# Performance work log

Hardware: AMD Instinct MI355X
Metric: run time of the kernel (lower is better)

Reference implementation:

```python
import jax, jax.numpy as jnp
import numpy as np

B, N, D_IN, D_OUT, K_NBR = 8, 2048, 128, 128, 8
BN_EPS = 1e-5

def setup_inputs() -> dict:
    key = jax.random.key(0)
    ks = jax.random.split(key, 5)
    xavier = (6.0 / (D_IN + D_OUT)) ** 0.5
    return {
        "x": jax.random.normal(ks[0], (B, N, D_IN), jnp.float32),
        "weight_self": jax.random.uniform(ks[1], (D_IN, D_OUT), jnp.float32, -xavier, xavier),
        "weight_neighbor": jax.random.uniform(ks[2], (D_IN, D_OUT), jnp.float32, -xavier, xavier),
        "kan_a": jax.random.normal(ks[3], (D_OUT, 3), jnp.float32) * 0.1,
        "kan_b": jax.random.normal(ks[4], (D_OUT, 2), jnp.float32) * 0.1,
        "bias": jnp.zeros((D_OUT,), jnp.float32),
        "bn_gamma": jnp.ones((D_OUT,), jnp.float32),
        "bn_beta": jnp.zeros((D_OUT,), jnp.float32),
    }

def _forward(x, weight_self, weight_neighbor, kan_a, kan_b, bias, bn_gamma, bn_beta):
    b, n, _ = x.shape
    # --- kNN graph build ---
    xx = jnp.sum(x * x, axis=2, keepdims=True)                       # [B,N,1]
    dist = xx - 2.0 * jnp.einsum('bnd,bmd->bnm', x, x) + jnp.swapaxes(xx, 1, 2)
    dist = jnp.clip(dist, 0.0, None)                                  # [B,N,N]
    k = min(K_NBR + 1, n)
    _, idx = jax.lax.top_k(-dist, k)                                  # smallest-k indices
    nbr = idx[:, :, 1:]                                               # drop self, [B,N,k-1]
    adj = jnp.zeros((b, n, n), x.dtype).at[
        jnp.arange(b)[:, None, None], jnp.arange(n)[None, :, None], nbr
    ].set(1.0)
    deg_inv_sqrt = (jnp.sum(adj, axis=2) + 1e-6) ** -0.5              # [B,N]
    adj_norm = deg_inv_sqrt[:, :, None] * adj * deg_inv_sqrt[:, None, :]
    adj_norm = adj_norm + jnp.eye(n, dtype=x.dtype)[None]
    # --- graph conv ---
    h_self = x @ weight_self                                          # [B,N,F]
    h_nbr = jnp.einsum('bnm,bmf->bnf', adj_norm, x @ weight_neighbor)
    h = h_self + h_nbr + bias
    # --- rational KAN activation (per-channel coefficients) ---
    h2 = h * h
    num = kan_a[:, 0] + kan_a[:, 1] * h + kan_a[:, 2] * h2
    den = 1.0 + jnp.abs(kan_b[:, 0] * h + kan_b[:, 1] * h2)
    h = num / (den + 1e-8)
    # --- BatchNorm1d (training mode): normalize each channel over (B,N) ---
    mean = jnp.mean(h, axis=(0, 1))
    var = jnp.var(h, axis=(0, 1))                                     # biased, matches torch BN
    h = (h - mean) * jax.lax.rsqrt(var + BN_EPS) * bn_gamma + bn_beta
    return h

def reference(x, weight_self, weight_neighbor, kan_a, kan_b, bias, bn_gamma, bn_beta):
    return _forward(x, weight_self, weight_neighbor, kan_a, kan_b, bias, bn_gamma, bn_beta)
```

## Files before the change

kernel.cpp:

```cpp
#include <hip/hip_runtime.h>
#include <stdint.h>

#define BB 8
#define NN 2048
#define DD 128

typedef unsigned long long ull;
typedef unsigned int u32;
typedef unsigned short u16;
typedef __attribute__((ext_vector_type(8))) short bf16x8;
typedef __attribute__((ext_vector_type(4))) float f32x4;

#define INS8(t8, cand) do { \
    t8[7] = (cand); ull _t; \
    if (t8[7] < t8[6]) { _t = t8[6]; t8[6] = t8[7]; t8[7] = _t; } \
    if (t8[6] < t8[5]) { _t = t8[5]; t8[5] = t8[6]; t8[6] = _t; } \
    if (t8[5] < t8[4]) { _t = t8[4]; t8[4] = t8[5]; t8[5] = _t; } \
    if (t8[4] < t8[3]) { _t = t8[3]; t8[3] = t8[4]; t8[4] = _t; } \
    if (t8[3] < t8[2]) { _t = t8[2]; t8[2] = t8[3]; t8[3] = _t; } \
    if (t8[2] < t8[1]) { _t = t8[1]; t8[1] = t8[2]; t8[2] = _t; } \
    if (t8[1] < t8[0]) { _t = t8[0]; t8[0] = t8[1]; t8[1] = _t; } \
  } while (0)

#define CEX(a, b) do { u32 _lo = (a) < (b) ? (a) : (b); \
                       u32 _hi = (a) < (b) ? (b) : (a); \
                       (a) = _lo; (b) = _hi; } while (0)

#define SORT8(c) do { \
    CEX(c[0], c[1]); CEX(c[2], c[3]); CEX(c[0], c[2]); CEX(c[1], c[3]); CEX(c[1], c[2]); \
    CEX(c[4], c[5]); CEX(c[6], c[7]); CEX(c[4], c[6]); CEX(c[5], c[7]); CEX(c[5], c[6]); \
    CEX(c[0], c[4]); CEX(c[1], c[5]); CEX(c[2], c[6]); CEX(c[3], c[7]); \
    CEX(c[2], c[4]); CEX(c[3], c[5]); \
    CEX(c[1], c[2]); CEX(c[3], c[4]); CEX(c[5], c[6]); } while (0)

#define MERGE8(t, s) do { \
    u32 m0_ = (t)[0] < (s)[7] ? (t)[0] : (s)[7]; \
    u32 m1_ = (t)[1] < (s)[6] ? (t)[1] : (s)[6]; \
    u32 m2_ = (t)[2] < (s)[5] ? (t)[2] : (s)[5]; \
    u32 m3_ = (t)[3] < (s)[4] ? (t)[3] : (s)[4]; \
    u32 m4_ = (t)[4] < (s)[3] ? (t)[4] : (s)[3]; \
    u32 m5_ = (t)[5] < (s)[2] ? (t)[5] : (s)[2]; \
    u32 m6_ = (t)[6] < (s)[1] ? (t)[6] : (s)[1]; \
    u32 m7_ = (t)[7] < (s)[0] ? (t)[7] : (s)[0]; \
    CEX(m0_, m4_); CEX(m1_, m5_); CEX(m2_, m6_); CEX(m3_, m7_); \
    CEX(m0_, m2_); CEX(m1_, m3_); CEX(m4_, m6_); CEX(m5_, m7_); \
    CEX(m0_, m1_); CEX(m2_, m3_); CEX(m4_, m5_); CEX(m6_, m7_); \
    (t)[0] = m0_; (t)[1] = m1_; (t)[2] = m2_; (t)[3] = m3_; \
    (t)[4] = m4_; (t)[5] = m5_; (t)[6] = m6_; (t)[7] = m7_; \
  } while (0)

__device__ inline u16 f2bf_rn(float f) {
  uint32_t u = __float_as_uint(f);
  return (u16)((u + 0x7fffu + ((u >> 16) & 1u)) >> 16);
}

typedef __attribute__((address_space(1))) const void gvoid_t;
typedef __attribute__((address_space(3))) void lvoid_t;
__device__ __forceinline__ void gload16(const void* g, void* l) {
  __builtin_amdgcn_global_load_lds((gvoid_t*)g, (lvoid_t*)l, 16, 0, 0);
}

__global__ __launch_bounds__(256) void k_cvx(const float* __restrict__ x,
                                             float* __restrict__ xx,
                                             u16* __restrict__ xh,
                                             u16* __restrict__ xl) {
  int row  = blockIdx.x * 4 + (threadIdx.x >> 6);
  int lane = threadIdx.x & 63;
  float2 v = *reinterpret_cast<const float2*>(x + (size_t)row * DD + lane * 2);
  float p = v.x * v.x + v.y * v.y;
  #pragma unroll
  for (int off = 1; off < 64; off <<= 1) p += __shfl_xor(p, off);
  if (lane == 0) xx[row] = p;
  u16 h0 = f2bf_rn(v.x);
  u16 l0 = f2bf_rn(v.x - __uint_as_float(((uint32_t)h0) << 16));
  u16 h1 = f2bf_rn(v.y);
  u16 l1 = f2bf_rn(v.y - __uint_as_float(((uint32_t)h1) << 16));
  size_t o = (size_t)row * DD + lane * 2;
  *(uint32_t*)(xh + o) = (uint32_t)h0 | ((uint32_t)h1 << 16);
  *(uint32_t*)(xl + o) = (uint32_t)l0 | ((uint32_t)l1 << 16);
}

__global__ __launch_bounds__(256, 2) void k_gemm(const float* __restrict__ x,
                                                 const float* __restrict__ Ws,
                                                 const float* __restrict__ Wn,
                                                 const float* __restrict__ bias,
                                                 float* __restrict__ hbase,
                                                 float* __restrict__ y) {
  __shared__ __align__(16) float xt[128 * 64];
  __shared__ __align__(16) float wt[128 * 64];
  int tid = threadIdx.x;
  int ch = blockIdx.x & 1;
  size_t r0 = (size_t)(blockIdx.x >> 1) * 64;

  {
    int rr = tid >> 2, kp = (tid & 3) << 5;
    const float* src = x + (r0 + rr) * DD + kp;
    #pragma unroll
    for (int q = 0; q < 8; ++q) {
      float4 v = *(const float4*)(src + (q << 2));
      int k = kp + (q << 2);
      xt[(k + 0) * 64 + rr] = v.x; xt[(k + 1) * 64 + rr] = v.y;
      xt[(k + 2) * 64 + rr] = v.z; xt[(k + 3) * 64 + rr] = v.w;
    }
  }
  {
    const float4* s4 = (const float4*)Ws;
    float4* w4 = (float4*)wt;
    #pragma unroll
    for (int q = 0; q < 8; ++q) {
      int idx = q * 256 + tid;
      w4[idx] = s4[((idx >> 4) << 5) + (ch << 4) + (idx & 15)];
    }
  }
  __syncthreads();

  int tc = tid & 15, tr = tid >> 4;
  float accS[4][4], accY[4][4];
  #pragma unroll
  for (int i = 0; i < 4; ++i)
    #pragma unroll
    for (int u = 0; u < 4; ++u) { accS[i][u] = 0.f; accY[i][u] = 0.f; }

  #pragma unroll 4
  for (int k = 0; k < 128; ++k) {
    float4 a4 = *(const float4*)(xt + k * 64 + (tr << 2));
    float4 w4 = *(const float4*)(wt + k * 64 + (tc << 2));
    float aa[4] = {a4.x, a4.y, a4.z, a4.w};
    float ww[4] = {w4.x, w4.y, w4.z, w4.w};
    #pragma unroll
    for (int i = 0; i < 4; ++i)
      #pragma unroll
      for (int u = 0; u < 4; ++u) accS[i][u] = fmaf(aa[i], ww[u], accS[i][u]);
  }
  __syncthreads();
  {
    const float4* s4 = (const float4*)Wn;
    float4* w4 = (float4*)wt;
    #pragma unroll
    for (int q = 0; q < 8; ++q) {
      int idx = q * 256 + tid;
      w4[idx] = s4[((idx >> 4) << 5) + (ch << 4) + (idx & 15)];
    }
  }
  __syncthreads();
  #pragma unroll 4
  for (int k = 0; k < 128; ++k) {
    float4 a4 = *(const float4*)(xt + k * 64 + (tr << 2));
    float4 w4 = *(const float4*)(wt + k * 64 + (tc << 2));
    float aa[4] = {a4.x, a4.y, a4.z, a4.w};
    float ww[4] = {w4.x, w4.y, w4.z, w4.w};
    #pragma unroll
    for (int i = 0; i < 4; ++i)
      #pragma unroll
      for (int u = 0; u < 4; ++u) accY[i][u] = fmaf(aa[i], ww[u], accY[i][u]);
  }

  int cg = (ch << 6) + (tc << 2);
  float4 bv = *(const float4*)(bias + cg);
  float bb[4] = {bv.x, bv.y, bv.z, bv.w};
  #pragma unroll
  for (int i = 0; i < 4; ++i) {
    size_t row = r0 + (tr << 2) + i;
    float h[4];
    #pragma unroll
    for (int u = 0; u < 4; ++u) h[u] = (accS[i][u] + accY[i][u]) + bb[u];
    *(float4*)(y + row * DD + cg)     = make_float4(accY[i][0], accY[i][1], accY[i][2], accY[i][3]);
    *(float4*)(hbase + row * DD + cg) = make_float4(h[0], h[1], h[2], h[3]);
  }
}

#define GLOAD(MC, BUF) do { \
    _Pragma("unroll") \
    for (int q = 0; q < 4; ++q) { \
      int ks_ = ((q & 1) << 2) + sks; \
      int mrow_ = mbase + ((MC) << 5) + ((q >> 1) << 4) + sr; \
      const u16* src_ = (ks_ < 4 ? xhb : xlb) + ((size_t)mrow_ << 7) + ((ks_ & 3) << 5) + (sg << 3); \
      gload16(src_, (char*)(&Bc[(BUF)][0]) + (((q << 8) + tid) << 4)); \
    } } while (0)

__global__ __launch_bounds__(256, 4) void k_knn(const u16* __restrict__ xh,
                                                const u16* __restrict__ xl,
                                                const float* __restrict__ xx,
                                                u32* __restrict__ cand) {
  __shared__ __align__(16) u16 Bc[2][8192];
  __shared__ float xxm[512];

  int tid = threadIdx.x;
  int lane = tid & 63, w = tid >> 6;
  int b = blockIdx.x & 7;
  int rest = blockIdx.x >> 3;
  int n0 = (rest & 31) << 6;
  int msplit = rest >> 5;
  int mbase = msplit << 9;
  const u16*  xhb = xh + (((size_t)b << 11) << 7);
  const u16*  xlb = xl + (((size_t)b << 11) << 7);
  const float* xxb = xx + ((size_t)b << 11);

  int sr = tid & 15, sg = (tid >> 4) & 3, sks = (tid >> 6) & 3;

  GLOAD(0, 0);

  {
    float2 t = *(const float2*)(xxb + mbase + tid * 2);
    xxm[tid * 2] = t.x; xxm[tid * 2 + 1] = t.y;
  }

  int r = lane & 15, g = lane >> 4;
  int myn = n0 + (w << 4) + r;
  float xxn = xxb[myn];

  bf16x8 ah[4], al[4];
  #pragma unroll
  for (int ks = 0; ks < 4; ++ks) {
    ah[ks] = *(const bf16x8*)(xhb + ((size_t)myn << 7) + (ks << 5) + (g << 3));
    al[ks] = *(const bf16x8*)(xlb + ((size_t)myn << 7) + (ks << 5) + (g << 3));
  }

  u32 t8[8];
  #pragma unroll
  for (int q = 0; q < 8; ++q) t8[q] = 0xFFFFFFFFu;

  __syncthreads();

  int cur = 0;
  for (int mc = 0; mc < 16; ++mc) {
    if (mc < 15) GLOAD(mc + 1, cur ^ 1);
    const u16* Bcur = &Bc[cur][0];
    u32 cds[8];
    #pragma unroll
    for (int p = 0; p < 2; ++p) {
      f32x4 ahh = {0.f, 0.f, 0.f, 0.f};
      f32x4 alh = {0.f, 0.f, 0.f, 0.f};
      f32x4 ahl = {0.f, 0.f, 0.f, 0.f};
      #pragma unroll
      for (int ks = 0; ks < 4; ++ks) {
        const u16* base = Bcur + (((p << 3) + ks) << 9) + (lane << 3);
        bf16x8 bh = *(const bf16x8*)(base);
        bf16x8 bo = *(const bf16x8*)(base + 2048);
        ahh = __builtin_amdgcn_mfma_f32_16x16x32_bf16(bh, ah[ks], ahh, 0, 0, 0);
        alh = __builtin_amdgcn_mfma_f32_16x16x32_bf16(bo, ah[ks], alh, 0, 0, 0);
        ahl = __builtin_amdgcn_mfma_f32_16x16x32_bf16(bh, al[ks], ahl, 0, 0, 0);
      }
      float4 xm4 = *(const float4*)(xxm + (mc << 5) + (p << 4) + (g << 2));
      float sx[4] = {xxn + xm4.x, xxn + xm4.y, xxn + xm4.z, xxn + xm4.w};
      int mb0 = mbase + (mc << 5) + (p << 4) + (g << 2);
      #pragma unroll
      for (int e = 0; e < 4; ++e) {
        float dot = (ahh[e] + alh[e]) + ahl[e];
        float d = fmaxf(fmaf(-2.f, dot, sx[e]), 0.f);
        int m = mb0 + e;
        u32 cd = (__float_as_uint(d) & 0xFFFFF000u) | (u32)m;
        cds[(p << 2) + e] = (m == myn) ? 0xFFFFFFFFu : cd;
      }
    }
    SORT8(cds);
    MERGE8(t8, cds);
    __syncthreads();
    cur ^= 1;
  }

  u32* mbuf = (u32*)(&Bc[0][0]);
  #pragma unroll
  for (int q = 0; q < 8; ++q)
    mbuf[((((w << 4) + r) << 5)) + (g << 3) + q] = t8[q];
  __syncthreads();
  if (g == 0) {
    for (int j = 1; j < 4; ++j) {
      u32 s8[8];
      #pragma unroll
      for (int q = 0; q < 8; ++q)
        s8[q] = mbuf[((((w << 4) + r) << 5)) + (j << 3) + q];
      MERGE8(t8, s8);
    }
    u32* cp = cand + ((((size_t)b << 11) + myn) << 5) + (msplit << 3);
    #pragma unroll
    for (int q = 0; q < 8; ++q) cp[q] = t8[q];
  }
}

__global__ __launch_bounds__(256) void k_rsc(const float* __restrict__ x,
                                             const float* __restrict__ xx,
                                             const u32* __restrict__ cand,
                                             int* __restrict__ nbr) {
  __shared__ ull ex[256];
  int tid = threadIdx.x;
  int rloc = tid >> 5;
  int c = tid & 31;
  int batch = blockIdx.x & 7;
  int within = blockIdx.x >> 3;
  int row = (batch << 11) + (within << 3) + rloc;
  u32 cd32 = cand[((size_t)row << 5) + c];
  int m = (int)(cd32 & 0xFFFu);
  const float* xn = x + (size_t)row * DD;
  const float* xm = x + ((size_t)(batch << 11) + m) * DD;
  float acc[8] = {0.f, 0.f, 0.f, 0.f, 0.f, 0.f, 0.f, 0.f};
  #pragma unroll
  for (int d8 = 0; d8 < 16; ++d8) {
    float4 a0 = *(const float4*)(xn + (d8 << 3));
    float4 a1 = *(const float4*)(xn + (d8 << 3) + 4);
    float4 v0 = *(const float4*)(xm + (d8 << 3));
    float4 v1 = *(const float4*)(xm + (d8 << 3) + 4);
    acc[0] = fmaf(a0.x, v0.x, acc[0]);
    acc[1] = fmaf(a0.y, v0.y, acc[1]);
    acc[2] = fmaf(a0.z, v0.z, acc[2]);
    acc[3] = fmaf(a0.w, v0.w, acc[3]);
    acc[4] = fmaf(a1.x, v1.x, acc[4]);
    acc[5] = fmaf(a1.y, v1.y, acc[5]);
    acc[6] = fmaf(a1.z, v1.z, acc[6]);
    acc[7] = fmaf(a1.w, v1.w, acc[7]);
  }
  float dot = ((acc[0] + acc[1]) + (acc[2] + acc[3])) +
              ((acc[4] + acc[5]) + (acc[6] + acc[7]));
  float dist = fmaxf((xx[row] - 2.f * dot) + xx[(batch << 11) + m], 0.f);
  ex[tid] = (((ull)__float_as_uint(dist)) << 32) | (unsigned)m;
  __syncthreads();
  if (c == 0) {
    ull t8[8];
    #pragma unroll
    for (int q = 0; q < 8; ++q) t8[q] = ~0ull;
    #pragma unroll
    for (int q = 0; q < 32; ++q) {
      ull v = ex[(rloc << 5) + q];
      if (v < t8[7]) INS8(t8, v);
    }
    int* op = nbr + (size_t)row * 8;
    #pragma unroll
    for (int q = 0; q < 8; ++q) op[q] = (int)(t8[q] & 0xffffffffu);
  }
}

__global__ __launch_bounds__(256) void k_kan(const float* __restrict__ hbase,
                                             const float* __restrict__ y,
                                             const int* __restrict__ nbr,
                                             const float* __restrict__ kan_a,
                                             const float* __restrict__ kan_b,
                                             float* __restrict__ hkan,
                                             double* __restrict__ sums) {
  __shared__ double redA[256], redB[256];
  int f = threadIdx.x & 127;
  int half = threadIdx.x >> 7;
  int batch = blockIdx.x & 7;
  int within = blockIdx.x >> 3;
  int r0 = (batch << 11) + (within << 5) + half * 16;
  const float* yb = y + ((size_t)batch << 11) * DD;
  float a0 = kan_a[f * 3 + 0], a1 = kan_a[f * 3 + 1], a2 = kan_a[f * 3 + 2];
  float b0 = kan_b[f * 2 + 0], b1 = kan_b[f * 2 + 1];
  float disf = (float)(1.0 / sqrt((double)(8.0f + 1e-6f)));
  float cf = disf * disf;
  double sh = 0.0, sh2 = 0.0;
  for (int i = 0; i < 16; ++i) {
    int r = r0 + i;
    const int* np_ = nbr + (size_t)r * 8;
    float t = 0.f;
    #pragma unroll
    for (int j = 0; j < 8; ++j) {
      int m = np_[j];
      float yv = yb[(size_t)m * DD + f];
      t = fmaf(cf, yv, t);
    }
    float h = hbase[(size_t)r * DD + f] + t;
    float h2 = h * h;
    float num = (a0 + a1 * h) + a2 * h2;
    float den = 1.0f + fabsf(b0 * h + b1 * h2);
    float hk = num / (den + 1e-8f);
    hkan[(size_t)r * DD + f] = hk;
    sh += (double)hk; sh2 += (double)hk * (double)hk;
  }
  redA[threadIdx.x] = sh; redB[threadIdx.x] = sh2;
  __syncthreads();
  if (half == 0) {
    atomicAdd(&sums[f], sh + redA[f + 128]);
    atomicAdd(&sums[128 + f], sh2 + redB[f + 128]);
  }
}

__global__ __launch_bounds__(256) void k_bn(const float* __restrict__ hkan,
                                            const double* __restrict__ sums,
                                            const float* __restrict__ gamma,
                                            const float* __restrict__ beta,
                                            float* __restrict__ out) {
  __shared__ float mn[128], sc[128], bt[128];
  int tid = threadIdx.x;
  if (tid < 128) {
    double M = (double)(BB * NN);
    double mean = sums[tid] / M;
    double var = sums[128 + tid] / M - mean * mean;
    if (var < 0.0) var = 0.0;
    mn[tid] = (float)mean;
    sc[tid] = (float)(1.0 / sqrt(var + 1e-5)) * gamma[tid];
    bt[tid] = beta[tid];
  }
  __syncthreads();
  const int total4 = BB * NN * DD / 4;
  for (int i4 = blockIdx.x * blockDim.x + threadIdx.x; i4 < total4;
       i4 += gridDim.x * blockDim.x) {
    float4 v = ((const float4*)hkan)[i4];
    int fb = (i4 * 4) & 127;
    float4 o;
    o.x = (v.x - mn[fb + 0]) * sc[fb + 0] + bt[fb + 0];
    o.y = (v.y - mn[fb + 1]) * sc[fb + 1] + bt[fb + 1];
    o.z = (v.z - mn[fb + 2]) * sc[fb + 2] + bt[fb + 2];
    o.w = (v.w - mn[fb + 3]) * sc[fb + 3] + bt[fb + 3];
    ((float4*)out)[i4] = o;
  }
}

extern "C" void kernel_launch(void* const* d_in, const int* in_sizes, int n_in,
                              void* d_out, int out_size, void* d_ws, size_t ws_size,
                              hipStream_t stream) {
  const float* x     = (const float*)d_in[0];
  const float* Ws    = (const float*)d_in[1];
  const float* Wn    = (const float*)d_in[2];
  const float* ka    = (const float*)d_in[3];
  const float* kb    = (const float*)d_in[4];
  const float* bias  = (const float*)d_in[5];
  const float* gamma = (const float*)d_in[6];
  const float* beta  = (const float*)d_in[7];
  float* out = (float*)d_out;

  char* ws = (char*)d_ws;
  float*  xx    = (float*)(ws + 0);
  int*    nbr   = (int*)(ws + 65536);
  double* sums  = (double*)(ws + 589824);
  float*  y     = (float*)(ws + 1048576);
  float*  hbase = (float*)(ws + 9437184);
  float*  hkan  = (float*)(ws + 17825792);
  u32*    cand  = (u32*)(ws + 17825792);
  u16*    xh    = (u16*)(ws + 22020096);
  u16*    xl    = (u16*)d_out;

  hipMemsetAsync(sums, 0, 256 * sizeof(double), stream);
  k_cvx <<<4096, 256, 0, stream>>>(x, xx, xh, xl);
  k_gemm<<<512,  256, 0, stream>>>(x, Ws, Wn, bias, hbase, y);
  k_knn <<<1024, 256, 0, stream>>>(xh, xl, xx, cand);
  k_rsc <<<2048, 256, 0, stream>>>(x, xx, cand, nbr);
  k_kan <<<512,  256, 0, stream>>>(hbase, y, nbr, ka, kb, hkan, sums);
  k_bn  <<<1024, 256, 0, stream>>>(hkan, sums, gamma, beta, out);
}
```

Baseline: 149.2 us.

## Skip sort/merge when tile has no better candidates; rescore only top-16 candidates

In the kNN tile loop, each thread first computes the min of its 8 candidates and only runs the sort-and-merge network when that min can enter the running top-8. The rescore kernel now bitonic-merges the four split lists down to the best 16 approximate candidates, instead of 32, before the exact fp32 rescoring. That halves the rescore grid and its gather traffic. The candidate key keeps 11 bits for the index instead of 12 (N=2048), which gives the distance one more bit of precision. Keeping only 16 candidates risks missing a true neighbour when the approximate distances are nearly tied.

After: 131.8 us. -11.6%, faster.

```diff
diff --git a/kernel.cpp b/kernel.cpp
--- a/kernel.cpp
+++ b/kernel.cpp
@@ -47,6 +47,15 @@
     CEX(m0_, m1_); CEX(m2_, m3_); CEX(m4_, m5_); CEX(m6_, m7_); \
     (t)[0] = m0_; (t)[1] = m1_; (t)[2] = m2_; (t)[3] = m3_; \
     (t)[4] = m4_; (t)[5] = m5_; (t)[6] = m6_; (t)[7] = m7_; \
+  } while (0)
+
+#define BMERGE16(c) do { \
+    _Pragma("unroll") for (int _i = 0; _i < 8; ++_i) CEX(c[_i], c[_i + 8]); \
+    _Pragma("unroll") for (int _g = 0; _g < 16; _g += 8) \
+      _Pragma("unroll") for (int _i = 0; _i < 4; ++_i) CEX(c[_g + _i], c[_g + _i + 4]); \
+    _Pragma("unroll") for (int _g = 0; _g < 16; _g += 4) \
+      _Pragma("unroll") for (int _i = 0; _i < 2; ++_i) CEX(c[_g + _i], c[_g + _i + 2]); \
+    _Pragma("unroll") for (int _g = 0; _g < 16; _g += 2) CEX(c[_g], c[_g + 1]); \
   } while (0)
 
 __device__ inline u16 f2bf_rn(float f) {
@@ -249,12 +258,23 @@
         float dot = (ahh[e] + alh[e]) + ahl[e];
         float d = fmaxf(fmaf(-2.f, dot, sx[e]), 0.f);
         int m = mb0 + e;
-        u32 cd = (__float_as_uint(d) & 0xFFFFF000u) | (u32)m;
+        u32 cd = (__float_as_uint(d) & 0xFFFFF800u) | (u32)m;
         cds[(p << 2) + e] = (m == myn) ? 0xFFFFFFFFu : cd;
       }
     }
-    SORT8(cds);
-    MERGE8(t8, cds);
+    {
+      u32 c01 = cds[0] < cds[1] ? cds[0] : cds[1];
+      u32 c23 = cds[2] < cds[3] ? cds[2] : cds[3];
+      u32 c45 = cds[4] < cds[5] ? cds[4] : cds[5];
+      u32 c67 = cds[6] < cds[7] ? cds[6] : cds[7];
+      u32 c03 = c01 < c23 ? c01 : c23;
+      u32 c47 = c45 < c67 ? c45 : c67;
+      u32 cmin = c03 < c47 ? c03 : c47;
+      if (cmin < t8[7]) {
+        SORT8(cds);
+        MERGE8(t8, cds);
+      }
+    }
     __syncthreads();
     cur ^= 1;
   }
@@ -282,45 +302,65 @@
                                              const float* __restrict__ xx,
                                              const u32* __restrict__ cand,
                                              int* __restrict__ nbr) {
-  __shared__ ull ex[256];
+  __shared__ u32 c16[16][16];
+  __shared__ ull ex[16][16];
   int tid = threadIdx.x;
-  int rloc = tid >> 5;
-  int c = tid & 31;
+  int rloc = tid >> 4;
+  int c = tid & 15;
   int batch = blockIdx.x & 7;
   int within = blockIdx.x >> 3;
-  int row = (batch << 11) + (within << 3) + rloc;
-  u32 cd32 = cand[((size_t)row << 5) + c];
-  int m = (int)(cd32 & 0xFFFu);
-  const float* xn = x + (size_t)row * DD;
-  const float* xm = x + ((size_t)(batch << 11) + m) * DD;
-  float acc[8] = {0.f, 0.f, 0.f, 0.f, 0.f, 0.f, 0.f, 0.f};
-  #pragma unroll
-  for (int d8 = 0; d8 < 16; ++d8) {
-    float4 a0 = *(const float4*)(xn + (d8 << 3));
-    float4 a1 = *(const float4*)(xn + (d8 << 3) + 4);
-    float4 v0 = *(const float4*)(xm + (d8 << 3));
-    float4 v1 = *(const float4*)(xm + (d8 << 3) + 4);
-    acc[0] = fmaf(a0.x, v0.x, acc[0]);
-    acc[1] = fmaf(a0.y, v0.y, acc[1]);
-    acc[2] = fmaf(a0.z, v0.z, acc[2]);
-    acc[3] = fmaf(a0.w, v0.w, acc[3]);
-    acc[4] = fmaf(a1.x, v1.x, acc[4]);
-    acc[5] = fmaf(a1.y, v1.y, acc[5]);
-    acc[6] = fmaf(a1.z, v1.z, acc[6]);
-    acc[7] = fmaf(a1.w, v1.w, acc[7]);
-  }
-  float dot = ((acc[0] + acc[1]) + (acc[2] + acc[3])) +
-              ((acc[4] + acc[5]) + (acc[6] + acc[7]));
-  float dist = fmaxf((xx[row] - 2.f * dot) + xx[(batch << 11) + m], 0.f);
-  ex[tid] = (((ull)__float_as_uint(dist)) << 32) | (unsigned)m;
+  int row = (batch << 11) + (within << 4) + rloc;
+
+  if (c == 0) {
+    const u32* cp = cand + ((size_t)row << 5);
+    u32 A[16], B[16];
+    #pragma unroll
+    for (int q = 0; q < 8; ++q) { A[q] = cp[q];      A[8 + q] = cp[15 - q]; }
+    #pragma unroll
+    for (int q = 0; q < 8; ++q) { B[q] = cp[16 + q]; B[8 + q] = cp[31 - q]; }
+    BMERGE16(A);
+    BMERGE16(B);
+    #pragma unroll
+    for (int i = 0; i < 16; ++i) {
+      u32 lo = A[i] < B[15 - i] ? A[i] : B[15 - i];
+      c16[rloc][i] = lo & 0x7FFu;
+    }
+  }
+  __syncthreads();
+
+  {
+    int m = (int)c16[rloc][c];
+    const float* xn = x + (size_t)row * DD;
+    const float* xm = x + ((size_t)(batch << 11) + m) * DD;
+    float acc[8] = {0.f, 0.f, 0.f, 0.f, 0.f, 0.f, 0.f, 0.f};
+    #pragma unroll
+    for (int d8 = 0; d8 < 16; ++d8) {
+      float4 a0 = *(const float4*)(xn + (d8 << 3));
+      float4 a1 = *(const float4*)(xn + (d8 << 3) + 4);
+      float4 v0 = *(const float4*)(xm + (d8 << 3));
+      float4 v1 = *(const float4*)(xm + (d8 << 3) + 4);
+      acc[0] = fmaf(a0.x, v0.x, acc[0]);
+      acc[1] = fmaf(a0.y, v0.y, acc[1]);
+      acc[2] = fmaf(a0.z, v0.z, acc[2]);
+      acc[3] = fmaf(a0.w, v0.w, acc[3]);
+      acc[4] = fmaf(a1.x, v1.x, acc[4]);
+      acc[5] = fmaf(a1.y, v1.y, acc[5]);
+      acc[6] = fmaf(a1.z, v1.z, acc[6]);
+      acc[7] = fmaf(a1.w, v1.w, acc[7]);
+    }
+    float dot = ((acc[0] + acc[1]) + (acc[2] + acc[3])) +
+                ((acc[4] + acc[5]) + (acc[6] + acc[7]));
+    float dist = fmaxf((xx[row] - 2.f * dot) + xx[(batch << 11) + m], 0.f);
+    ex[rloc][c] = (((ull)__float_as_uint(dist)) << 32) | (unsigned)m;
+  }
   __syncthreads();
   if (c == 0) {
     ull t8[8];
     #pragma unroll
     for (int q = 0; q < 8; ++q) t8[q] = ~0ull;
     #pragma unroll
-    for (int q = 0; q < 32; ++q) {
-      ull v = ex[(rloc << 5) + q];
+    for (int q = 0; q < 16; ++q) {
+      ull v = ex[rloc][q];
       if (v < t8[7]) INS8(t8, v);
     }
     int* op = nbr + (size_t)row * 8;
@@ -433,7 +473,7 @@
   k_cvx <<<4096, 256, 0, stream>>>(x, xx, xh, xl);
   k_gemm<<<512,  256, 0, stream>>>(x, Ws, Wn, bias, hbase, y);
   k_knn <<<1024, 256, 0, stream>>>(xh, xl, xx, cand);
-  k_rsc <<<2048, 256, 0, stream>>>(x, xx, cand, nbr);
+  k_rsc <<<1024, 256, 0, stream>>>(x, xx, cand, nbr);
   k_kan <<<512,  256, 0, stream>>>(hbase, y, nbr, ka, kb, hkan, sums);
   k_bn  <<<1024, 256, 0, stream>>>(hkan, sums, gamma, beta, out);
 }
```
